# Kernel tuning notes

Measured on AMD Instinct MI355X. Metric: run time of the kernel, lower is better.

The kernel has to match this reference:

```python
import jax, jax.numpy as jnp
import numpy as np

N = 16384   # num nodes
E = 524288  # num edges (avg degree 32)
C = 128     # in_channels == hidden_channels (residual requires equality)


def setup_inputs() -> dict:
    key = jax.random.key(0)
    ks = jax.random.split(key, 16)
    s = 1.0 / np.sqrt(C)  # glorot-ish scale
    return {
        "x": jax.random.normal(ks[0], (N, C), dtype=jnp.float32),
        "edge_index": jax.random.randint(ks[1], (2, E), 0, N, dtype=jnp.int32),
        "edge_attr": jax.random.normal(ks[2], (E, 8), dtype=jnp.float32),
        # GATConv 1 params
        "W1": jax.random.normal(ks[3], (C, C), dtype=jnp.float32) * s,
        "a_src1": jax.random.normal(ks[4], (C,), dtype=jnp.float32) * s,
        "a_dst1": jax.random.normal(ks[5], (C,), dtype=jnp.float32) * s,
        "b1": jnp.zeros((C,), dtype=jnp.float32),
        # GATConv 2 params
        "W2": jax.random.normal(ks[6], (C, C), dtype=jnp.float32) * s,
        "a_src2": jax.random.normal(ks[7], (C,), dtype=jnp.float32) * s,
        "a_dst2": jax.random.normal(ks[8], (C,), dtype=jnp.float32) * s,
        "b2": jnp.zeros((C,), dtype=jnp.float32),
        # TemporalAttention params
        "att_weight": jax.random.normal(ks[9], (C, C), dtype=jnp.float32) * s,
        "att_bias": jnp.zeros((C,), dtype=jnp.float32),
        # LayerNorm params
        "ln_gamma": jnp.ones((C,), dtype=jnp.float32),
        "ln_beta": jnp.zeros((C,), dtype=jnp.float32),
    }


def _gat_conv(x, edge_index, W, a_src, a_dst, b):
    """PyG GATConv, heads=1, negative_slope=0.2, add_self_loops=True.
    Edge (j -> i): src = edge_index[0], dst = edge_index[1]; softmax over dst."""
    n = x.shape[0]
    xw = x @ W                                   # [N, C]
    loops = jnp.arange(n, dtype=edge_index.dtype)
    src = jnp.concatenate([edge_index[0], loops])  # [E+N]
    dst = jnp.concatenate([edge_index[1], loops])
    alpha_src = xw @ a_src                       # [N]
    alpha_dst = xw @ a_dst                       # [N]
    e = jax.nn.leaky_relu(alpha_src[src] + alpha_dst[dst], negative_slope=0.2)
    # numerically stable segment softmax over destination nodes
    e_max = jax.ops.segment_max(e, dst, num_segments=n)
    p = jnp.exp(e - e_max[dst])
    denom = jax.ops.segment_sum(p, dst, num_segments=n)
    alpha = p / denom[dst]                       # [E+N]
    out = jax.ops.segment_sum(alpha[:, None] * xw[src], dst, num_segments=n)
    return out + b


def reference(x, edge_index, edge_attr, W1, a_src1, a_dst1, b1,
              W2, a_src2, a_dst2, b2, att_weight, att_bias, ln_gamma, ln_beta):
    # edge_attr is accepted but unused: GATConv was built without edge_dim,
    # so PyG ignores it in the attention computation.
    h = jax.nn.relu(_gat_conv(x, edge_index, W1, a_src1, a_dst1, b1))
    # dropout p=0.2 is identity in eval mode
    h = _gat_conv(h, edge_index, W2, a_src2, a_dst2, b2)

    # TemporalAttention over the (batch=1, N, C) view -> dense NxN attention
    q = h @ att_weight                            # [N, C]
    scores = (q @ h.T) / jnp.sqrt(jnp.float32(h.shape[-1]))  # [N, N]
    attn = jax.nn.softmax(scores, axis=-1)
    h = attn @ h + att_bias                       # [N, C]

    h = h + x                                     # residual
    mu = jnp.mean(h, axis=-1, keepdims=True)
    var = jnp.var(h, axis=-1, keepdims=True)
    h = (h - mu) / jnp.sqrt(var + 1e-5) * ln_gamma + ln_beta
    return h
```

## Files before the change

### kernel.cpp

```cpp
#include <hip/hip_runtime.h>

#define CC 128

typedef __attribute__((ext_vector_type(8))) short bf16x8;
typedef __attribute__((ext_vector_type(16))) float f32x16;

static __device__ __forceinline__ float lrelu(float v){ return v > 0.f ? v : 0.2f*v; }
static __device__ __forceinline__ unsigned short f2bf(float f){
  unsigned u = __float_as_uint(f);
  unsigned r = (u + 0x7fffu + ((u >> 16) & 1u)) >> 16;
  return (unsigned short)r;
}
static __device__ __forceinline__ float bf2f(unsigned short s){
  return __uint_as_float(((unsigned)s) << 16);
}
static __device__ __forceinline__ float bf2f_lo(unsigned u){
  return __uint_as_float(u << 16);
}
static __device__ __forceinline__ float bf2f_hi(unsigned u){
  return __uint_as_float(u & 0xffff0000u);
}
static __device__ __forceinline__ unsigned cvtpk(float lo, float hi){
  unsigned r;
  asm("v_cvt_pk_bf16_f32 %0, %1, %2" : "=v"(r) : "v"(lo), "v"(hi));
  return r;
}

#define QSCALE (0.08838834764831845f * 1.4426950408889634f)
#define L2E 1.4426950408889634f

#if defined(__has_builtin)
#if __has_builtin(__builtin_amdgcn_global_load_lds)
#define HAVE_GLL 1
#endif
#endif

#ifdef HAVE_GLL
static __device__ __forceinline__ void gload_lds16(const uint4* g, uint4* l){
  __builtin_amdgcn_global_load_lds(
      (const __attribute__((address_space(1))) unsigned int*)(const void*)g,
      (__attribute__((address_space(3))) unsigned int*)(void*)l, 16, 0, 0);
}
#endif

__global__ __launch_bounds__(256) void pack_w3(const float* __restrict__ W1,
                                               const float* __restrict__ W2,
                                               const float* __restrict__ Wa,
                                               unsigned short* __restrict__ img){
  int gid = blockIdx.x*256 + threadIdx.x;
  int m = gid >> 11, u = gid & 2047;
  const float* W = (m==0) ? W1 : (m==1) ? W2 : Wa;
  int k = u >> 8, ct = (u >> 6) & 3, l = u & 63;
  int h = l >> 5, c = ct*32 + (l & 31);
  int k0 = k*16 + h*8;
  float f[8];
  #pragma unroll
  for (int j=0;j<8;j++) f[j] = W[(k0+j)*CC + c];
  uint4 o;
  o.x = cvtpk(f[0],f[1]); o.y = cvtpk(f[2],f[3]);
  o.z = cvtpk(f[4],f[5]); o.w = cvtpk(f[6],f[7]);
  *(uint4*)&img[((size_t)m*2048 + u)*8] = o;
}

template<bool ABF16, int OMODE>
__global__ __launch_bounds__(256) void gemm_mfma(const void* __restrict__ Av,
                                                 const uint4* __restrict__ Wimg,
                                                 unsigned short* __restrict__ out){
  __shared__ uint4 WS[2048];
  const int tid = threadIdx.x, lane = tid & 63, w = tid >> 6;
  const int h = lane >> 5, l31 = lane & 31;
  const long r0 = (long)blockIdx.x * 64;
#ifdef HAVE_GLL
  #pragma unroll
  for (int i=0;i<8;i++){ int u = i*256 + w*64; gload_lds16(Wimg + u + lane, &WS[u]); }
#else
  #pragma unroll
  for (int i=0;i<8;i++){ int u = i*256 + tid; WS[u] = Wimg[u]; }
#endif
  const int rt = w & 1, ct0 = (w >> 1) * 2;
  const long arow = (r0 + rt*32 + l31)*CC + h*8;
  f32x16 acc0 = {}, acc1 = {};
  __syncthreads();
  #pragma unroll
  for (int k=0;k<8;k++){
    bf16x8 afr;
    if (ABF16){
      afr = *(const bf16x8*)&((const unsigned short*)Av)[arow + k*16];
    } else {
      const float* ap = (const float*)Av + arow + k*16;
      float4 a0 = *(const float4*)ap;
      float4 a1 = *(const float4*)(ap+4);
      uint4 av;
      av.x = cvtpk(a0.x,a0.y); av.y = cvtpk(a0.z,a0.w);
      av.z = cvtpk(a1.x,a1.y); av.w = cvtpk(a1.z,a1.w);
      __builtin_memcpy(&afr, &av, 16);
    }
    bf16x8 b0 = *(const bf16x8*)&WS[(k*4+ct0  )*64 + lane];
    bf16x8 b1 = *(const bf16x8*)&WS[(k*4+ct0+1)*64 + lane];
    acc0 = __builtin_amdgcn_mfma_f32_32x32x16_bf16(afr, b0, acc0, 0,0,0);
    acc1 = __builtin_amdgcn_mfma_f32_32x32x16_bf16(afr, b1, acc1, 0,0,0);
  }
  #pragma unroll
  for (int r=0;r<16;r++){
    long row = r0 + rt*32 + (r&3) + 8*(r>>2) + 4*h;
    float s0 = (OMODE==1) ? acc0[r]*QSCALE : acc0[r];
    float s1 = (OMODE==1) ? acc1[r]*QSCALE : acc1[r];
    out[row*CC + ct0*32 + l31]     = f2bf(s0);
    out[row*CC + (ct0+1)*32 + l31] = f2bf(s1);
  }
}

__global__ __launch_bounds__(256) void rowdot2b(const unsigned short* __restrict__ X,
                                                const float* __restrict__ a1,
                                                const float* __restrict__ a2,
                                                float* __restrict__ as_, float* __restrict__ ad_){
  const int lane = threadIdx.x & 63;
  const long row = (long)blockIdx.x*4 + (threadIdx.x >> 6);
  unsigned u = *(const unsigned*)&X[row*CC + lane*2];
  float v0 = bf2f_lo(u);
  float v1 = bf2f_hi(u);
  float2 w1 = ((const float2*)a1)[lane];
  float2 w2 = ((const float2*)a2)[lane];
  float s1 = v0*w1.x + v1*w1.y;
  float s2 = v0*w2.x + v1*w2.y;
  #pragma unroll
  for (int off=32; off; off>>=1){
    s1 += __shfl_xor(s1, off);
    s2 += __shfl_xor(s2, off);
  }
  if (lane==0){ as_[row]=s1; ad_[row]=s2; }
}

__global__ void zero_int(int* __restrict__ p, int n){
  int i = blockIdx.x*256 + threadIdx.x;
  if (i < n) p[i] = 0;
}
__global__ void csr_hist(const int* __restrict__ ei, int* __restrict__ deg, int E){
  int e = blockIdx.x*256 + threadIdx.x;
  if (e < E) atomicAdd(&deg[ei[E + e]], 1);
}
__global__ __launch_bounds__(256) void csr_scan(const int* __restrict__ deg,
                                                int* __restrict__ rowptr,
                                                int* __restrict__ cursor, int N){
  __shared__ int part[257];
  const int t = threadIdx.x;
  const int per = N / 256;
  const int base = t*per;
  int s = 0;
  for (int j=0;j<per;j++) s += deg[base+j];
  part[t+1] = s;
  if (t==0) part[0] = 0;
  __syncthreads();
  if (t==0){
    for (int i=1;i<=256;i++) part[i] += part[i-1];
  }
  __syncthreads();
  int run = part[t];
  for (int j=0;j<per;j++){
    rowptr[base+j] = run;
    cursor[base+j] = run;
    run += deg[base+j];
  }
  if (t==255) rowptr[N] = run;
}
__global__ void csr_fill(const int* __restrict__ ei, int* __restrict__ cursor,
                         int* __restrict__ csrc, int E){
  int e = blockIdx.x*256 + threadIdx.x;
  if (e < E){
    int d = ei[E + e];
    int slot = atomicAdd(&cursor[d], 1);
    csrc[slot] = ei[e];
  }
}

template<bool RELUOUT>
__global__ __launch_bounds__(256) void gat_gather(
    const int* __restrict__ rowptr, const int* __restrict__ csrc,
    const float* __restrict__ as_, const float* __restrict__ ad_,
    const unsigned short* __restrict__ X, const float* __restrict__ b,
    unsigned short* __restrict__ O, int N){
  const int lane = threadIdx.x & 63;
  const int g = lane >> 4, l16 = lane & 15;
  const int dst = blockIdx.x*4 + (threadIdx.x >> 6);
  const float adv = ad_[dst];
  float m = lrelu(as_[dst] + adv);
  float l = 1.f;
  float acc[8] = {0.f,0.f,0.f,0.f,0.f,0.f,0.f,0.f};
  if (g == 0){
    uint4 v = *(const uint4*)&X[(size_t)dst*CC + l16*8];
    acc[0]=bf2f_lo(v.x); acc[1]=bf2f_hi(v.x);
    acc[2]=bf2f_lo(v.y); acc[3]=bf2f_hi(v.y);
    acc[4]=bf2f_lo(v.z); acc[5]=bf2f_hi(v.z);
    acc[6]=bf2f_lo(v.w); acc[7]=bf2f_hi(v.w);
  }
  const int kb = rowptr[dst];
  const int deg = rowptr[dst+1] - kb;
  for (int c0 = 0; c0 < deg; c0 += 64){
    const int nv = min(64, deg - c0);
    int src = dst; float e = -3.0e38f;
    if (lane < nv){
      src = csrc[kb + c0 + lane];
      e = lrelu(as_[src] + adv);
    }
    float cm = e;
    #pragma unroll
    for (int off=32; off; off>>=1) cm = fmaxf(cm, __shfl_xor(cm, off));
    if (cm > m){
      float fr = __builtin_amdgcn_exp2f((m - cm)*L2E);
      l *= fr;
      #pragma unroll
      for (int k=0;k<8;k++) acc[k] *= fr;
      m = cm;
    }
    float p = __builtin_amdgcn_exp2f((e - m)*L2E);
    float cs = p;
    #pragma unroll
    for (int off=32; off; off>>=1) cs += __shfl_xor(cs, off);
    l += cs;
    for (int j = 0; j < nv; j += 4){
      int idx = j + g;
      float w_e = __shfl(p, idx);
      int   s_e = __shfl(src, idx);
      uint4 v = *(const uint4*)&X[(size_t)s_e*CC + l16*8];
      acc[0] += w_e*bf2f_lo(v.x); acc[1] += w_e*bf2f_hi(v.x);
      acc[2] += w_e*bf2f_lo(v.y); acc[3] += w_e*bf2f_hi(v.y);
      acc[4] += w_e*bf2f_lo(v.z); acc[5] += w_e*bf2f_hi(v.z);
      acc[6] += w_e*bf2f_lo(v.w); acc[7] += w_e*bf2f_hi(v.w);
    }
  }
  #pragma unroll
  for (int k=0;k<8;k++){
    acc[k] += __shfl_xor(acc[k], 16);
    acc[k] += __shfl_xor(acc[k], 32);
  }
  if (g == 0){
    float inv = 1.f / l;
    float4 b0 = *(const float4*)&b[l16*8];
    float4 b1 = *(const float4*)&b[l16*8 + 4];
    float r0 = acc[0]*inv + b0.x, r1 = acc[1]*inv + b0.y;
    float r2 = acc[2]*inv + b0.z, r3 = acc[3]*inv + b0.w;
    float r4 = acc[4]*inv + b1.x, r5 = acc[5]*inv + b1.y;
    float r6 = acc[6]*inv + b1.z, r7 = acc[7]*inv + b1.w;
    if (RELUOUT){
      r0=fmaxf(r0,0.f); r1=fmaxf(r1,0.f); r2=fmaxf(r2,0.f); r3=fmaxf(r3,0.f);
      r4=fmaxf(r4,0.f); r5=fmaxf(r5,0.f); r6=fmaxf(r6,0.f); r7=fmaxf(r7,0.f);
    }
    uint4 o;
    o.x = cvtpk(r0,r1); o.y = cvtpk(r2,r3);
    o.z = cvtpk(r4,r5); o.w = cvtpk(r6,r7);
    *(uint4*)&O[(size_t)dst*CC + l16*8] = o;
  }
}

template<int NKT>
__global__ __launch_bounds__(256) void convert_pack(const unsigned short* __restrict__ h,
                                                    uint4* __restrict__ IMG, int N){
  const int KVB = NKT*32;
  int idx = blockIdx.x*256 + threadIdx.x;
  int tile = idx / (NKT*1024);
  int u = idx - tile*(NKT*1024);
  int l = u & 63, hh = l >> 5, l31 = l & 31;
  if (u < NKT*512){
    int kt = u >> 9, ks = (u >> 6) & 7;
    int key = tile*KVB + kt*32 + l31;
    IMG[idx] = *(const uint4*)&h[(size_t)key*CC + ks*16 + hh*8];
  } else {
    int v = u - NKT*512;
    int ks = (v >> 6) & (2*NKT - 1);
    int ct = v >> (NKT==1 ? 7 : 8);
    int c = ct*32 + l31;
    int key0 = tile*KVB + ks*16 + hh*8;
    unsigned short o[8];
    #pragma unroll
    for (int j=0;j<8;j++) o[j] = h[(size_t)(key0+j)*CC + c];
    IMG[idx] = *(uint4*)o;
  }
}

template<int NKT, int NQT>
__global__ __launch_bounds__(256,2) void attn_mfma(
    const unsigned short* __restrict__ Qb, const uint4* __restrict__ IMG,
    unsigned short* __restrict__ opW, float* __restrict__ ml, int N, int nsplit){
  const int TILE4 = NKT*1024;
  __shared__ uint4 SH[2*NKT*1024];

  const int tid = threadIdx.x;
  const int lane = tid & 63, w = tid >> 6;
  const int h = lane >> 5, q31 = lane & 31;
  const int flat = blockIdx.x;
  const int split = flat % nsplit;
  const int qb0 = (flat / nsplit) * (128*NQT);
  const int KVB = NKT*32;
  const int ntt = N / KVB;
  const int tb = (ntt*split)/nsplit, te = (ntt*(split+1))/nsplit;

  int qrow[NQT];
  bf16x8 qf[NQT][8];
  #pragma unroll
  for (int qt=0; qt<NQT; qt++){
    qrow[qt] = qb0 + w*(32*NQT) + qt*32 + q31;
    #pragma unroll
    for (int ks=0; ks<8; ks++)
      qf[qt][ks] = *(const bf16x8*)&Qb[(size_t)qrow[qt]*CC + ks*16 + h*8];
  }

  f32x16 zero16 = {};
  f32x16 acc_o[4][NQT];
  #pragma unroll
  for (int ct=0; ct<4; ct++)
    #pragma unroll
    for (int qt=0; qt<NQT; qt++) acc_o[ct][qt] = zero16;
  float m_[NQT], l_[NQT];
  #pragma unroll
  for (int qt=0; qt<NQT; qt++){ m_[qt] = -3.0e38f; l_[qt] = 0.f; }

  int cur = 0;
  {
    const uint4* src = IMG + (size_t)tb*TILE4;
#ifdef HAVE_GLL
    #pragma unroll
    for (int i=0;i<NKT*4;i++){ int u = i*256 + w*64; gload_lds16(src + u + lane, &SH[u]); }
#else
    #pragma unroll
    for (int i=0;i<NKT*4;i++){ int u = i*256 + tid; SH[u] = src[u]; }
#endif
  }

  for (int t=tb; t<te; t++){
    __syncthreads();
    if (t+1 < te){
      const uint4* src = IMG + (size_t)(t+1)*TILE4;
      uint4* dst = &SH[(cur^1)*TILE4];
#ifdef HAVE_GLL
      #pragma unroll
      for (int i=0;i<NKT*4;i++){ int u = i*256 + w*64; gload_lds16(src + u + lane, dst + u); }
#else
      #pragma unroll
      for (int i=0;i<NKT*4;i++){ int u = i*256 + tid; dst[u] = src[u]; }
#endif
    }
    const uint4* B = &SH[cur*TILE4];

    f32x16 accs[NKT][NQT];
    #pragma unroll
    for (int kt=0; kt<NKT; kt++){
      #pragma unroll
      for (int qt=0; qt<NQT; qt++) accs[kt][qt] = zero16;
      __builtin_amdgcn_s_setprio(1);
      #pragma unroll
      for (int ks=0; ks<8; ks++){
        bf16x8 hf = *(const bf16x8*)&B[(kt*8+ks)*64 + lane];
        #pragma unroll
        for (int qt=0; qt<NQT; qt++)
          accs[kt][qt] = __builtin_amdgcn_mfma_f32_32x32x16_bf16(hf, qf[qt][ks], accs[kt][qt], 0,0,0);
      }
      __builtin_amdgcn_s_setprio(0);
    }

    float tm[NQT];
    #pragma unroll
    for (int qt=0; qt<NQT; qt++){
      float tmax[16];
      #pragma unroll
      for (int r=0;r<16;r++){
        float v = accs[0][qt][r];
        if (NKT == 2) v = fmaxf(v, accs[1][qt][r]);
        tmax[r] = v;
      }
      #pragma unroll
      for (int s=8; s; s>>=1)
        #pragma unroll
        for (int r=0;r<s;r++) tmax[r] = fmaxf(tmax[r], tmax[r+s]);
      tm[qt] = fmaxf(tmax[0], __shfl_xor(tmax[0], 32));
    }
    bool ok = true;
    #pragma unroll
    for (int qt=0; qt<NQT; qt++) ok &= (tm[qt] <= m_[qt] + 11.0f);
    if (!__all(ok)){
      #pragma unroll
      for (int qt=0; qt<NQT; qt++){
        float mn = fmaxf(m_[qt], tm[qt]);
        float fr = __builtin_amdgcn_exp2f(m_[qt] - mn);
        m_[qt] = mn; l_[qt] *= fr;
        #pragma unroll
        for (int ct=0; ct<4; ct++)
          #pragma unroll
          for (int r=0;r<16;r++) acc_o[ct][qt][r] *= fr;
      }
    }
    unsigned pk[NQT][NKT][8];
    #pragma unroll
    for (int qt=0; qt<NQT; qt++){
      float psum[16];
      #pragma unroll
      for (int kt=0; kt<NKT; kt++)
        #pragma unroll
        for (int r=0;r<16;r++)
          accs[kt][qt][r] = __builtin_amdgcn_exp2f(accs[kt][qt][r] - m_[qt]);
      #pragma unroll
      for (int r=0;r<16;r++){
        float v = accs[0][qt][r];
        if (NKT == 2) v += accs[1][qt][r];
        psum[r] = v;
      }
      #pragma unroll
      for (int s=8; s; s>>=1)
        #pragma unroll
        for (int r=0;r<s;r++) psum[r] += psum[r+s];
      l_[qt] += psum[0] + __shfl_xor(psum[0], 32);
      #pragma unroll
      for (int kt=0; kt<NKT; kt++)
        #pragma unroll
        for (int wd=0; wd<8; wd++)
          pk[qt][kt][wd] = cvtpk(accs[kt][qt][2*wd], accs[kt][qt][2*wd+1]);
    }

    #pragma unroll
    for (int ks=0; ks<2*NKT; ks++){
      const int kt = ks >> 1, W = (ks & 1)*4;
      bf16x8 pfrag[NQT];
      #pragma unroll
      for (int qt=0; qt<NQT; qt++){
        unsigned w0o = pk[qt][kt][W+0], w1o = pk[qt][kt][W+1];
        unsigned w2o = pk[qt][kt][W+2], w3o = pk[qt][kt][W+3];
        unsigned va = h ? w0o : w2o;
        unsigned vb = h ? w1o : w3o;
        unsigned fa = (unsigned)__shfl_xor((int)va, 32);
        unsigned fb = (unsigned)__shfl_xor((int)vb, 32);
        uint4 fw;
        fw.x = h ? fa : w0o;
        fw.y = h ? fb : w1o;
        fw.z = h ? w2o : fa;
        fw.w = h ? w3o : fb;
        __builtin_memcpy(&pfrag[qt], &fw, 16);
      }
      __builtin_amdgcn_s_setprio(1);
      #pragma unroll
      for (int ct=0; ct<4; ct++){
        bf16x8 hf = *(const bf16x8*)&B[NKT*512 + (ct*2*NKT+ks)*64 + lane];
        #pragma unroll
        for (int qt=0; qt<NQT; qt++)
          acc_o[ct][qt] = __builtin_amdgcn_mfma_f32_32x32x16_bf16(hf, pfrag[qt], acc_o[ct][qt], 0,0,0);
      }
      __builtin_amdgcn_s_setprio(0);
    }
    cur ^= 1;
  }

  #pragma unroll
  for (int qt=0; qt<NQT; qt++){
    float inv = 1.f / l_[qt];
    unsigned apk[4][8];
    #pragma unroll
    for (int ct=0; ct<4; ct++)
      #pragma unroll
      for (int wd=0; wd<8; wd++)
        apk[ct][wd] = cvtpk(acc_o[ct][qt][2*wd]*inv, acc_o[ct][qt][2*wd+1]*inv);

    unsigned short* orow = opW + (size_t)split*N*CC + (size_t)qrow[qt]*CC + h*64;
    #pragma unroll
    for (int cp=0; cp<2; cp++){
      #pragma unroll
      for (int jp=0; jp<4; jp++){
        int wd0 = 2*jp, wd1 = 2*jp+1;
        unsigned a0 = apk[cp][wd0],   a1 = apk[cp][wd1];
        unsigned b0 = apk[cp+2][wd0], b1 = apk[cp+2][wd1];
        unsigned v0 = h ? a0 : b0;
        unsigned v1 = h ? a1 : b1;
        unsigned f0 = (unsigned)__shfl_xor((int)v0, 32);
        unsigned f1 = (unsigned)__shfl_xor((int)v1, 32);
        unsigned o0 = h ? b0 : a0;
        unsigned o1 = h ? b1 : a1;
        uint4 st;
        st.x = h ? f0 : o0;
        st.y = h ? f1 : o1;
        st.z = h ? o0 : f0;
        st.w = h ? o1 : f1;
        *(uint4*)&orow[cp*32 + jp*8] = st;
      }
    }
    if (lane < 32)
      ((float2*)ml)[(size_t)split*N + qrow[qt]] = make_float2(m_[qt], l_[qt]);
  }
}

template<int NS>
__global__ __launch_bounds__(256) void merge_ln(
    const unsigned short* __restrict__ opW, const float* __restrict__ ml,
    const float* __restrict__ x, const float* __restrict__ ab,
    const float* __restrict__ gam, const float* __restrict__ bet,
    float* __restrict__ out, int N){
  const int lane = threadIdx.x & 63;
  const long row = (long)blockIdx.x*4 + (threadIdx.x >> 6);
  float mm[NS], ll[NS];
  float M = -3.0e38f;
  #pragma unroll
  for (int i=0;i<NS;i++){
    float2 v = ((const float2*)ml)[(size_t)i*N + row];
    mm[i]=v.x; ll[i]=v.y;
    M = fmaxf(M, v.x);
  }
  float den = 0.f;
  float wgt[NS];
  #pragma unroll
  for (int i=0;i<NS;i++){ wgt[i] = exp2f(mm[i]-M)*ll[i]; den += wgt[i]; }
  float invd = 1.f/den;
  float o0 = 0.f, o1 = 0.f;
  #pragma unroll
  for (int i=0;i<NS;i++){
    unsigned u = *(const unsigned*)&opW[((size_t)i*N + row)*CC + lane*2];
    float c = wgt[i]*invd;
    o0 += c * bf2f_lo(u);
    o1 += c * bf2f_hi(u);
  }
  float2 xb = ((const float2*)(x + row*CC))[lane];
  float2 bb = ((const float2*)ab)[lane];
  float a0 = o0 + bb.x + xb.x;
  float a1 = o1 + bb.y + xb.y;
  float s = a0 + a1, ss = a0*a0 + a1*a1;
  #pragma unroll
  for (int off=32; off; off>>=1){ s += __shfl_xor(s,off); ss += __shfl_xor(ss,off); }
  float mu  = s * (1.f/128.f);
  float var = ss * (1.f/128.f) - mu*mu;
  float rstd = rsqrtf(var + 1e-5f);
  float2 gg = ((const float2*)gam)[lane];
  float2 b2 = ((const float2*)bet)[lane];
  float2 r;
  r.x = (a0 - mu)*rstd*gg.x + b2.x;
  r.y = (a1 - mu)*rstd*gg.y + b2.y;
  ((float2*)(out + row*CC))[lane] = r;
}

extern "C" void kernel_launch(void* const* d_in, const int* in_sizes, int n_in,
                              void* d_out, int out_size, void* d_ws, size_t ws_size,
                              hipStream_t stream) {
  const float* x   = (const float*)d_in[0];
  const int*   ei  = (const int*)d_in[1];
  const float* W1  = (const float*)d_in[3];
  const float* a_s1= (const float*)d_in[4];
  const float* a_d1= (const float*)d_in[5];
  const float* b1  = (const float*)d_in[6];
  const float* W2  = (const float*)d_in[7];
  const float* a_s2= (const float*)d_in[8];
  const float* a_d2= (const float*)d_in[9];
  const float* b2  = (const float*)d_in[10];
  const float* Wa  = (const float*)d_in[11];
  const float* ab  = (const float*)d_in[12];
  const float* g   = (const float*)d_in[13];
  const float* be  = (const float*)d_in[14];
  float* out = (float*)d_out;

  const int N = in_sizes[0] / CC;
  const int E = in_sizes[1] / 2;
  const size_t MB = 1024*1024;
  const size_t KB = 1024;

  char* base = (char*)d_ws;
  uint4* IMG  = (uint4*)(base);
  unsigned short* xwb = (unsigned short*)(base + 8*MB);
  unsigned short* hW  = (unsigned short*)(base + 12*MB);
  int* csrc   = (int*)(base + 16*MB);
  int* rowptr = (int*)(base + 18*MB);
  int* cursor = (int*)(base + 18*MB + 128*KB);
  int* deg    = (int*)(base + 18*MB + 256*KB);
  float* as_  = (float*)(base + 18*MB + 384*KB);
  float* ad_  = (float*)(base + 18*MB + 512*KB);
  unsigned short* Wimg = (unsigned short*)(base + 19*MB);
  unsigned short* opW  = (unsigned short*)(base + 8*MB);
  unsigned short* QbD  = (unsigned short*)d_out;

  const uint4* W1i = (const uint4*)(Wimg);
  const uint4* W2i = (const uint4*)(Wimg + 2048*8);
  const uint4* Wai = (const uint4*)(Wimg + 2*2048*8);

  int ns;
  if (ws_size >= 74*MB)      ns = 16;
  else if (ws_size >= 41*MB) ns = 8;
  else                       ns = 4;
  float* ml = (float*)(base + 8*MB + (size_t)ns*4*MB);

  dim3 B(256);

  pack_w3<<<24, B, 0, stream>>>(W1, W2, Wa, Wimg);
  zero_int<<<(N+255)/256, B, 0, stream>>>(deg, N);
  csr_hist<<<(E+255)/256, B, 0, stream>>>(ei, deg, E);
  csr_scan<<<1, B, 0, stream>>>(deg, rowptr, cursor, N);
  csr_fill<<<(E+255)/256, B, 0, stream>>>(ei, cursor, csrc, E);

  gemm_mfma<false,0><<<N/64, B, 0, stream>>>(x, W1i, xwb);
  rowdot2b<<<N/4, B, 0, stream>>>(xwb, a_s1, a_d1, as_, ad_);
  gat_gather<true><<<N/4, B, 0, stream>>>(rowptr, csrc, as_, ad_, xwb, b1, hW, N);

  gemm_mfma<true,0><<<N/64, B, 0, stream>>>(hW, W2i, xwb);
  rowdot2b<<<N/4, B, 0, stream>>>(xwb, a_s2, a_d2, as_, ad_);
  gat_gather<false><<<N/4, B, 0, stream>>>(rowptr, csrc, as_, ad_, xwb, b2, hW, N);

  gemm_mfma<true,1><<<N/64, B, 0, stream>>>(hW, Wai, QbD);
  if (ns >= 8){
    convert_pack<1><<<(N*32)/256, B, 0, stream>>>(hW, IMG, N);
    attn_mfma<1,2><<<(N/256)*ns, B, 0, stream>>>(QbD, IMG, opW, ml, N, ns);
    if (ns == 16)
      merge_ln<16><<<N/4, B, 0, stream>>>(opW, ml, x, ab, g, be, out, N);
    else
      merge_ln<8><<<N/4, B, 0, stream>>>(opW, ml, x, ab, g, be, out, N);
  } else {
    convert_pack<2><<<(N*32)/256, B, 0, stream>>>(hW, IMG, N);
    attn_mfma<2,1><<<(N/128)*4, B, 0, stream>>>(QbD, IMG, opW, ml, N, 4);
    merge_ln<4><<<N/4, B, 0, stream>>>(opW, ml, x, ab, g, be, out, N);
  }
}
```

Before: 323.8 us.

## Stream K/V tiles directly into registers instead of LDS double-buffering

Replaces the LDS double-buffered attention kernel with one where each wave loads the packed key/value tile image straight from global memory into registers, ping-ponging between two register buffers across tiles. This removes the shared-memory staging and the per-tile __syncthreads. In exchange, all four waves in a block fetch the same tile separately from global/L2, and register pressure goes up. The loop steps two tiles at a time and loads tile t+1 unconditionally, so an odd tile count per split would read past the range. The NKT=2 variant and its dispatch path are removed.

```diff
diff --git a/kernel.cpp b/kernel.cpp
--- a/kernel.cpp
+++ b/kernel.cpp
@@ -10,9 +10,6 @@
   unsigned u = __float_as_uint(f);
   unsigned r = (u + 0x7fffu + ((u >> 16) & 1u)) >> 16;
   return (unsigned short)r;
-}
-static __device__ __forceinline__ float bf2f(unsigned short s){
-  return __uint_as_float(((unsigned)s) << 16);
 }
 static __device__ __forceinline__ float bf2f_lo(unsigned u){
   return __uint_as_float(u << 16);
@@ -252,24 +249,22 @@
   }
 }
 
-template<int NKT>
 __global__ __launch_bounds__(256) void convert_pack(const unsigned short* __restrict__ h,
                                                     uint4* __restrict__ IMG, int N){
-  const int KVB = NKT*32;
   int idx = blockIdx.x*256 + threadIdx.x;
-  int tile = idx / (NKT*1024);
-  int u = idx - tile*(NKT*1024);
+  int tile = idx >> 10;
+  int u = idx & 1023;
   int l = u & 63, hh = l >> 5, l31 = l & 31;
-  if (u < NKT*512){
-    int kt = u >> 9, ks = (u >> 6) & 7;
-    int key = tile*KVB + kt*32 + l31;
+  if (u < 512){
+    int ks = u >> 6;
+    int key = tile*32 + l31;
     IMG[idx] = *(const uint4*)&h[(size_t)key*CC + ks*16 + hh*8];
   } else {
-    int v = u - NKT*512;
-    int ks = (v >> 6) & (2*NKT - 1);
-    int ct = v >> (NKT==1 ? 7 : 8);
+    int v = u - 512;
+    int ks = (v >> 6) & 1;
+    int ct = v >> 7;
     int c = ct*32 + l31;
-    int key0 = tile*KVB + ks*16 + hh*8;
+    int key0 = tile*32 + ks*16 + hh*8;
     unsigned short o[8];
     #pragma unroll
     for (int j=0;j<8;j++) o[j] = h[(size_t)(key0+j)*CC + c];
@@ -277,185 +272,158 @@
   }
 }
 
-template<int NKT, int NQT>
-__global__ __launch_bounds__(256,2) void attn_mfma(
+static __device__ __forceinline__ void attn_step(
+    const uint4 (&A)[16], const bf16x8 (&qf)[2][8],
+    f32x16 (&acc_o0)[4], f32x16 (&acc_o1)[4],
+    float (&m_)[2], float (&l_)[2], int h){
+  f32x16 accs[2] = {};
+  __builtin_amdgcn_s_setprio(1);
+  #pragma unroll
+  for (int ks=0; ks<8; ks++){
+    bf16x8 hf;
+    __builtin_memcpy(&hf, &A[ks], 16);
+    accs[0] = __builtin_amdgcn_mfma_f32_32x32x16_bf16(hf, qf[0][ks], accs[0], 0,0,0);
+    accs[1] = __builtin_amdgcn_mfma_f32_32x32x16_bf16(hf, qf[1][ks], accs[1], 0,0,0);
+  }
+  __builtin_amdgcn_s_setprio(0);
+
+  float tm[2];
+  #pragma unroll
+  for (int qt=0; qt<2; qt++){
+    float tmax[16];
+    #pragma unroll
+    for (int r=0;r<16;r++) tmax[r] = accs[qt][r];
+    #pragma unroll
+    for (int s=8; s; s>>=1)
+      #pragma unroll
+      for (int r=0;r<s;r++) tmax[r] = fmaxf(tmax[r], tmax[r+s]);
+    tm[qt] = fmaxf(tmax[0], __shfl_xor(tmax[0], 32));
+  }
+  bool ok = (tm[0] <= m_[0] + 11.0f) & (tm[1] <= m_[1] + 11.0f);
+  if (!__all(ok)){
+    #pragma unroll
+    for (int qt=0; qt<2; qt++){
+      float mn = fmaxf(m_[qt], tm[qt]);
+      float fr = __builtin_amdgcn_exp2f(m_[qt] - mn);
+      m_[qt] = mn; l_[qt] *= fr;
+      #pragma unroll
+      for (int ct=0; ct<4; ct++)
+        #pragma unroll
+        for (int r=0;r<16;r++){
+          acc_o0[ct][r] = (qt==0) ? acc_o0[ct][r]*fr : acc_o0[ct][r];
+          acc_o1[ct][r] = (qt==1) ? acc_o1[ct][r]*fr : acc_o1[ct][r];
+        }
+    }
+  }
+  unsigned pk[2][8];
+  #pragma unroll
+  for (int qt=0; qt<2; qt++){
+    #pragma unroll
+    for (int r=0;r<16;r++)
+      accs[qt][r] = __builtin_amdgcn_exp2f(accs[qt][r] - m_[qt]);
+    float ps[16];
+    #pragma unroll
+    for (int r=0;r<16;r++) ps[r] = accs[qt][r];
+    #pragma unroll
+    for (int s=8; s; s>>=1)
+      #pragma unroll
+      for (int r=0;r<s;r++) ps[r] += ps[r+s];
+    l_[qt] += ps[0] + __shfl_xor(ps[0], 32);
+    #pragma unroll
+    for (int wd=0; wd<8; wd++)
+      pk[qt][wd] = cvtpk(accs[qt][2*wd], accs[qt][2*wd+1]);
+  }
+
+  #pragma unroll
+  for (int ks=0; ks<2; ks++){
+    const int W = ks*4;
+    bf16x8 pf0, pf1;
+    #pragma unroll
+    for (int qt=0; qt<2; qt++){
+      unsigned w0o = pk[qt][W+0], w1o = pk[qt][W+1];
+      unsigned w2o = pk[qt][W+2], w3o = pk[qt][W+3];
+      unsigned va = h ? w0o : w2o;
+      unsigned vb = h ? w1o : w3o;
+      unsigned fa = (unsigned)__shfl_xor((int)va, 32);
+      unsigned fb = (unsigned)__shfl_xor((int)vb, 32);
+      uint4 fw;
+      fw.x = h ? fa : w0o;
+      fw.y = h ? fb : w1o;
+      fw.z = h ? w2o : fa;
+      fw.w = h ? w3o : fb;
+      if (qt==0) __builtin_memcpy(&pf0, &fw, 16);
+      else       __builtin_memcpy(&pf1, &fw, 16);
+    }
+    __builtin_amdgcn_s_setprio(1);
+    #pragma unroll
+    for (int ct=0; ct<4; ct++){
+      bf16x8 hf;
+      __builtin_memcpy(&hf, &A[8 + ct*2 + ks], 16);
+      acc_o0[ct] = __builtin_amdgcn_mfma_f32_32x32x16_bf16(hf, pf0, acc_o0[ct], 0,0,0);
+      acc_o1[ct] = __builtin_amdgcn_mfma_f32_32x32x16_bf16(hf, pf1, acc_o1[ct], 0,0,0);
+    }
+    __builtin_amdgcn_s_setprio(0);
+  }
+}
+
+__global__ __launch_bounds__(256) void attn_reg(
     const unsigned short* __restrict__ Qb, const uint4* __restrict__ IMG,
     unsigned short* __restrict__ opW, float* __restrict__ ml, int N, int nsplit){
-  const int TILE4 = NKT*1024;
-  __shared__ uint4 SH[2*NKT*1024];
-
   const int tid = threadIdx.x;
   const int lane = tid & 63, w = tid >> 6;
   const int h = lane >> 5, q31 = lane & 31;
   const int flat = blockIdx.x;
   const int split = flat % nsplit;
-  const int qb0 = (flat / nsplit) * (128*NQT);
-  const int KVB = NKT*32;
-  const int ntt = N / KVB;
+  const int qb0 = (flat / nsplit) * 256;
+  const int ntt = N >> 5;
   const int tb = (ntt*split)/nsplit, te = (ntt*(split+1))/nsplit;
 
-  int qrow[NQT];
-  bf16x8 qf[NQT][8];
-  #pragma unroll
-  for (int qt=0; qt<NQT; qt++){
-    qrow[qt] = qb0 + w*(32*NQT) + qt*32 + q31;
+  int qrow[2];
+  bf16x8 qf[2][8];
+  #pragma unroll
+  for (int qt=0; qt<2; qt++){
+    qrow[qt] = qb0 + w*64 + qt*32 + q31;
     #pragma unroll
     for (int ks=0; ks<8; ks++)
       qf[qt][ks] = *(const bf16x8*)&Qb[(size_t)qrow[qt]*CC + ks*16 + h*8];
   }
 
-  f32x16 zero16 = {};
-  f32x16 acc_o[4][NQT];
-  #pragma unroll
-  for (int ct=0; ct<4; ct++)
-    #pragma unroll
-    for (int qt=0; qt<NQT; qt++) acc_o[ct][qt] = zero16;
-  float m_[NQT], l_[NQT];
-  #pragma unroll
-  for (int qt=0; qt<NQT; qt++){ m_[qt] = -3.0e38f; l_[qt] = 0.f; }
-
-  int cur = 0;
+  f32x16 acc_o0[4] = {}, acc_o1[4] = {};
+  float m_[2] = {-3.0e38f, -3.0e38f};
+  float l_[2] = {0.f, 0.f};
+
+  uint4 A0[16], A1[16];
   {
-    const uint4* src = IMG + (size_t)tb*TILE4;
-#ifdef HAVE_GLL
-    #pragma unroll
-    for (int i=0;i<NKT*4;i++){ int u = i*256 + w*64; gload_lds16(src + u + lane, &SH[u]); }
-#else
-    #pragma unroll
-    for (int i=0;i<NKT*4;i++){ int u = i*256 + tid; SH[u] = src[u]; }
-#endif
-  }
-
-  for (int t=tb; t<te; t++){
-    __syncthreads();
-    if (t+1 < te){
-      const uint4* src = IMG + (size_t)(t+1)*TILE4;
-      uint4* dst = &SH[(cur^1)*TILE4];
-#ifdef HAVE_GLL
-      #pragma unroll
-      for (int i=0;i<NKT*4;i++){ int u = i*256 + w*64; gload_lds16(src + u + lane, dst + u); }
-#else
-      #pragma unroll
-      for (int i=0;i<NKT*4;i++){ int u = i*256 + tid; dst[u] = src[u]; }
-#endif
-    }
-    const uint4* B = &SH[cur*TILE4];
-
-    f32x16 accs[NKT][NQT];
-    #pragma unroll
-    for (int kt=0; kt<NKT; kt++){
-      #pragma unroll
-      for (int qt=0; qt<NQT; qt++) accs[kt][qt] = zero16;
-      __builtin_amdgcn_s_setprio(1);
-      #pragma unroll
-      for (int ks=0; ks<8; ks++){
-        bf16x8 hf = *(const bf16x8*)&B[(kt*8+ks)*64 + lane];
-        #pragma unroll
-        for (int qt=0; qt<NQT; qt++)
-          accs[kt][qt] = __builtin_amdgcn_mfma_f32_32x32x16_bf16(hf, qf[qt][ks], accs[kt][qt], 0,0,0);
-      }
-      __builtin_amdgcn_s_setprio(0);
-    }
-
-    float tm[NQT];
-    #pragma unroll
-    for (int qt=0; qt<NQT; qt++){
-      float tmax[16];
-      #pragma unroll
-      for (int r=0;r<16;r++){
-        float v = accs[0][qt][r];
-        if (NKT == 2) v = fmaxf(v, accs[1][qt][r]);
-        tmax[r] = v;
-      }
-      #pragma unroll
-      for (int s=8; s; s>>=1)
-        #pragma unroll
-        for (int r=0;r<s;r++) tmax[r] = fmaxf(tmax[r], tmax[r+s]);
-      tm[qt] = fmaxf(tmax[0], __shfl_xor(tmax[0], 32));
-    }
-    bool ok = true;
-    #pragma unroll
-    for (int qt=0; qt<NQT; qt++) ok &= (tm[qt] <= m_[qt] + 11.0f);
-    if (!__all(ok)){
-      #pragma unroll
-      for (int qt=0; qt<NQT; qt++){
-        float mn = fmaxf(m_[qt], tm[qt]);
-        float fr = __builtin_amdgcn_exp2f(m_[qt] - mn);
-        m_[qt] = mn; l_[qt] *= fr;
-        #pragma unroll
-        for (int ct=0; ct<4; ct++)
-          #pragma unroll
-          for (int r=0;r<16;r++) acc_o[ct][qt][r] *= fr;
-      }
-    }
-    unsigned pk[NQT][NKT][8];
-    #pragma unroll
-    for (int qt=0; qt<NQT; qt++){
-      float psum[16];
-      #pragma unroll
-      for (int kt=0; kt<NKT; kt++)
-        #pragma unroll
-        for (int r=0;r<16;r++)
-          accs[kt][qt][r] = __builtin_amdgcn_exp2f(accs[kt][qt][r] - m_[qt]);
-      #pragma unroll
-      for (int r=0;r<16;r++){
-        float v = accs[0][qt][r];
-        if (NKT == 2) v += accs[1][qt][r];
-        psum[r] = v;
-      }
-      #pragma unroll
-      for (int s=8; s; s>>=1)
-        #pragma unroll
-        for (int r=0;r<s;r++) psum[r] += psum[r+s];
-      l_[qt] += psum[0] + __shfl_xor(psum[0], 32);
-      #pragma unroll
-      for (int kt=0; kt<NKT; kt++)
-        #pragma unroll
-        for (int wd=0; wd<8; wd++)
-          pk[qt][kt][wd] = cvtpk(accs[kt][qt][2*wd], accs[kt][qt][2*wd+1]);
-    }
-
-    #pragma unroll
-    for (int ks=0; ks<2*NKT; ks++){
-      const int kt = ks >> 1, W = (ks & 1)*4;
-      bf16x8 pfrag[NQT];
-      #pragma unroll
-      for (int qt=0; qt<NQT; qt++){
-        unsigned w0o = pk[qt][kt][W+0], w1o = pk[qt][kt][W+1];
-        unsigned w2o = pk[qt][kt][W+2], w3o = pk[qt][kt][W+3];
-        unsigned va = h ? w0o : w2o;
-        unsigned vb = h ? w1o : w3o;
-        unsigned fa = (unsigned)__shfl_xor((int)va, 32);
-        unsigned fb = (unsigned)__shfl_xor((int)vb, 32);
-        uint4 fw;
-        fw.x = h ? fa : w0o;
-        fw.y = h ? fb : w1o;
-        fw.z = h ? w2o : fa;
-        fw.w = h ? w3o : fb;
-        __builtin_memcpy(&pfrag[qt], &fw, 16);
-      }
-      __builtin_amdgcn_s_setprio(1);
-      #pragma unroll
-      for (int ct=0; ct<4; ct++){
-        bf16x8 hf = *(const bf16x8*)&B[NKT*512 + (ct*2*NKT+ks)*64 + lane];
-        #pragma unroll
-        for (int qt=0; qt<NQT; qt++)
-          acc_o[ct][qt] = __builtin_amdgcn_mfma_f32_32x32x16_bf16(hf, pfrag[qt], acc_o[ct][qt], 0,0,0);
-      }
-      __builtin_amdgcn_s_setprio(0);
-    }
-    cur ^= 1;
-  }
-
-  #pragma unroll
-  for (int qt=0; qt<NQT; qt++){
+    const uint4* p = IMG + (size_t)tb*1024 + lane;
+    #pragma unroll
+    for (int i=0;i<16;i++) A0[i] = p[i*64];
+  }
+
+  for (int t=tb; t<te; t+=2){
+    {
+      const uint4* p = IMG + (size_t)(t+1)*1024 + lane;
+      #pragma unroll
+      for (int i=0;i<16;i++) A1[i] = p[i*64];
+    }
+    attn_step(A0, qf, acc_o0, acc_o1, m_, l_, h);
+    if (t+2 < te){
+      const uint4* p = IMG + (size_t)(t+2)*1024 + lane;
+      #pragma unroll
+      for (int i=0;i<16;i++) A0[i] = p[i*64];
+    }
+    attn_step(A1, qf, acc_o0, acc_o1, m_, l_, h);
+  }
+
+  #pragma unroll
+  for (int qt=0; qt<2; qt++){
     float inv = 1.f / l_[qt];
     unsigned apk[4][8];
     #pragma unroll
     for (int ct=0; ct<4; ct++)
       #pragma unroll
       for (int wd=0; wd<8; wd++)
-        apk[ct][wd] = cvtpk(acc_o[ct][qt][2*wd]*inv, acc_o[ct][qt][2*wd+1]*inv);
+        apk[ct][wd] = (qt==0) ? cvtpk(acc_o0[ct][2*wd]*inv, acc_o0[ct][2*wd+1]*inv)
+                              : cvtpk(acc_o1[ct][2*wd]*inv, acc_o1[ct][2*wd+1]*inv);
 
     unsigned short* orow = opW + (size_t)split*N*CC + (size_t)qrow[qt]*CC + h*64;
     #pragma unroll
@@ -596,16 +564,13 @@
   gat_gather<false><<<N/4, B, 0, stream>>>(rowptr, csrc, as_, ad_, xwb, b2, hW, N);
 
   gemm_mfma<true,1><<<N/64, B, 0, stream>>>(hW, Wai, QbD);
-  if (ns >= 8){
-    convert_pack<1><<<(N*32)/256, B, 0, stream>>>(hW, IMG, N);
-    attn_mfma<1,2><<<(N/256)*ns, B, 0, stream>>>(QbD, IMG, opW, ml, N, ns);
-    if (ns == 16)
-      merge_ln<16><<<N/4, B, 0, stream>>>(opW, ml, x, ab, g, be, out, N);
-    else
-      merge_ln<8><<<N/4, B, 0, stream>>>(opW, ml, x, ab, g, be, out, N);
-  } else {
-    convert_pack<2><<<(N*32)/256, B, 0, stream>>>(hW, IMG, N);
-    attn_mfma<2,1><<<(N/128)*4, B, 0, stream>>>(QbD, IMG, opW, ml, N, 4);
+  convert_pack<<<(N*32)/256, B, 0, stream>>>(hW, IMG, N);
+  attn_reg<<<(N/256)*ns, B, 0, stream>>>(QbD, IMG, opW, ml, N, ns);
+
+  if (ns == 16)
+    merge_ln<16><<<N/4, B, 0, stream>>>(opW, ml, x, ab, g, be, out, N);
+  else if (ns == 8)
+    merge_ln<8><<<N/4, B, 0, stream>>>(opW, ml, x, ab, g, be, out, N);
+  else
     merge_ln<4><<<N/4, B, 0, stream>>>(opW, ml, x, ab, g, be, out, N);
-  }
-}
+}
```

Result: slower. 498.6 us (+54.0%).
